# Performance work log

Measured on AMD Instinct MI355X. Metric: run time of the kernel, lower is better.

Reference implementation:

```python
import jax, jax.numpy as jnp
import numpy as np

B, S, H, HEADS, STEP = 128, 256, 128, 8, 1


def setup_inputs() -> dict:
    key = jax.random.key(0)
    ks = jax.random.split(key, 20)
    rn = lambda k, shape: jax.random.normal(k, shape, dtype=jnp.float32) * 0.1
    return {
        "A": jax.random.uniform(ks[0], (B, S, 2 * S), dtype=jnp.float32),
        "hidden": jax.random.normal(ks[1], (B, S, H), dtype=jnp.float32),
        "mask": jnp.ones((B, S), dtype=jnp.int32),
        "w_ih": rn(ks[2], (3 * H, 2 * H)),
        "w_hh": rn(ks[3], (3 * H, H)),
        "b_ih": rn(ks[4], (3 * H,)),
        "b_hh": rn(ks[5], (3 * H,)),
        "b_iah": rn(ks[6], (H,)),
        "b_oah": rn(ks[7], (H,)),
        "W_ein": rn(ks[8], (H, H)), "b_ein": rn(ks[9], (H,)),
        "W_eout": rn(ks[10], (H, H)), "b_eout": rn(ks[11], (H,)),
        "W_q0": rn(ks[12], (H, H)), "b_q0": rn(ks[13], (H,)),
        "W_q1": rn(ks[14], (H, H)), "b_q1": rn(ks[15], (H,)),
        "W_q2": rn(ks[16], (H, H)), "b_q2": rn(ks[17], (H,)),
    }


def _forward(A, hidden, mask, w_ih, w_hh, b_ih, b_hh, b_iah, b_oah,
             W_ein, b_ein, W_eout, b_eout, W_q0, b_q0, W_q1, b_q1, W_q2, b_q2):
    b, s, h = hidden.shape
    dk = h // HEADS
    # ---- GNN: gated graph propagation (GRU cell over adjacency messages) ----
    for _ in range(STEP):
        msg_in = A[:, :, :s] @ (hidden @ W_ein.T + b_ein) + b_iah    # [B,S,H]
        msg_out = A[:, :, s:] @ (hidden @ W_eout.T + b_eout) + b_oah  # [B,S,H]
        inputs = jnp.concatenate([msg_in, msg_out], axis=2)           # [B,S,2H]
        gi = inputs @ w_ih.T + b_ih                                   # [B,S,3H]
        gh = hidden @ w_hh.T + b_hh                                   # [B,S,3H]
        i_r, i_i, i_n = jnp.split(gi, 3, axis=2)
        h_r, h_i, h_n = jnp.split(gh, 3, axis=2)
        resetgate = jax.nn.sigmoid(i_r + h_r)
        inputgate = jax.nn.sigmoid(i_i + h_i)
        newgate = jnp.tanh(i_n + resetgate * h_n)
        hidden = hidden - inputgate * (hidden - newgate)
    # ---- query: hidden state of the last valid item in each session ----
    last_idx = jnp.sum(mask, axis=1) - 1
    ht1 = hidden[jnp.arange(b), last_idx]                             # [B,H]
    # ---- LastAttenion: sigmoid score + double softmax readout ----
    q0 = (ht1 @ W_q0.T + b_q0).reshape(b, HEADS, dk)                  # [B,h,dk]
    q1 = (hidden @ W_q1.T + b_q1).reshape(b, s, HEADS, dk).transpose(0, 2, 1, 3)
    q2 = (hidden @ W_q2.T + b_q2).reshape(b, s, HEADS, dk).transpose(0, 2, 1, 3)
    # q0 is expanded over the query axis, so every score row is identical
    alpha = jax.nn.sigmoid(jnp.einsum('bhd,bhjd->bhj', q0, q1))        # [B,h,S]
    alpha = jnp.broadcast_to(alpha[:, :, None, :], (b, HEADS, s, s))   # [B,h,S,S]
    alpha = jax.nn.softmax(alpha, axis=-1)
    row_keep = (mask > 0)[:, None, :, None]                            # [B,1,S,1]
    alpha = jnp.where(row_keep, alpha, -jnp.inf)
    alpha = jax.nn.softmax(2.0 * alpha, axis=1)                        # over heads
    alpha = jnp.where(row_keep, alpha, 0.0)  # guard fully-masked rows (torch would NaN)
    x = jnp.einsum('bhij,bhjd->bhid', alpha, q2)                       # [B,h,S,dk]
    x = x.transpose(0, 2, 1, 3).reshape(b, s, h)                       # [B,S,H]
    a = jnp.sum(x * mask[:, :, None].astype(x.dtype), axis=1)          # [B,H]
    return a


def reference(A, hidden, mask, w_ih, w_hh, b_ih, b_hh, b_iah, b_oah,
              W_ein, b_ein, W_eout, b_eout, W_q0, b_q0, W_q1, b_q1, W_q2, b_q2):
    return _forward(A, hidden, mask, w_ih, w_hh, b_ih, b_hh, b_iah, b_oah,
                    W_ein, b_ein, W_eout, b_eout, W_q0, b_q0, W_q1, b_q1, W_q2, b_q2)
```

## Files before the change

kernel.cpp:

```cpp
#include <hip/hip_runtime.h>
#include <cstdint>
#include <cstddef>

#define BB   128
#define SS   256
#define HH   128
#define NH   8
#define DKK  16

typedef unsigned short u16;
typedef __attribute__((ext_vector_type(8))) short   sh8;
typedef __attribute__((ext_vector_type(4))) float   f32x4;

__device__ __forceinline__ float sigmoidf_(float x) { return 1.f / (1.f + expf(-x)); }

__device__ __forceinline__ u16 f2bf(float x) {
    union { float f; unsigned int u; } v; v.f = x;
    unsigned int r = (v.u + 0x7fffu + ((v.u >> 16) & 1u)) >> 16;
    return (u16)r;
}
__device__ __forceinline__ float bf2f(u16 u) {
    union { unsigned int u; float f; } v; v.u = ((unsigned int)u) << 16;
    return v.f;
}
__device__ __forceinline__ float bflo(unsigned u) {
    union { unsigned u; float f; } v; v.u = u << 16; return v.f;
}
__device__ __forceinline__ float bfhi(unsigned u) {
    union { unsigned u; float f; } v; v.u = u & 0xffff0000u; return v.f;
}

#define BKk 32
#define PK  40

template<int XMODE, int OMODE>
__global__ __launch_bounds__(256) void gemm_mfma(
    const void* __restrict__ Xa, const void* __restrict__ Xc, int ldx, int ldx1, int ksplit,
    long long sXb, long long sXh,
    const u16* __restrict__ Bw, int ldb, long long sBb, long long sBh,
    const float* __restrict__ bias,
    void* __restrict__ Out, long long ldo, long long sOb, long long sOh,
    int K, const u16* __restrict__ hid)
{
    __shared__ __align__(16) char smem[2 * 128 * PK * 2];
    u16* As = (u16*)smem;
    u16* Bs = (u16*)(smem + 128 * PK * 2);

    const int t  = threadIdx.x;
    const int bm = blockIdx.x * 128;
    const int bn = blockIdx.y * 128;
    const long long zb = blockIdx.z >> 1, zh = blockIdx.z & 1;

    const u16* Bp = Bw + zb * sBb + zh * sBh;

    const int wave = t >> 6, lane = t & 63;
    const int wr = (wave >> 1) * 64, wc = (wave & 1) * 64;
    const int fm = lane & 15, fq = lane >> 4;

    f32x4 acc[4][4] = {};

    const int r0  = t >> 2, kk0 = (t & 3) * 8;
    const int r1  = t >> 3, kk1 = (t & 7) * 4;

    uint4  px0, px1, pb0, pb1;
    float4 pf0, pf1, pf2, pf3;

#define LOADX(K0)                                                                    \
    if (XMODE == 1) {                                                                \
        const float* Xf_ = (const float*)Xa + zb * sXb + zh * sXh;                   \
        const float* xp_ = Xf_ + (long long)(bm + r1) * ldx + (K0) + kk1;            \
        pf0 = *(const float4*)(xp_);                                                 \
        pf1 = *(const float4*)(xp_ + 32LL * ldx);                                    \
        pf2 = *(const float4*)(xp_ + 64LL * ldx);                                    \
        pf3 = *(const float4*)(xp_ + 96LL * ldx);                                    \
    } else if (XMODE == 2 && (K0) >= ksplit) {                                       \
        const u16* xp_ = (const u16*)Xc + (long long)(bm + r0) * ldx1                \
                         + ((K0) - ksplit) + kk0;                                    \
        px0 = *(const uint4*)(xp_);                                                  \
        px1 = *(const uint4*)(xp_ + 64LL * ldx1);                                    \
    } else {                                                                         \
        const u16* xp_ = (const u16*)Xa + (long long)(bm + r0) * ldx + (K0) + kk0;   \
        px0 = *(const uint4*)(xp_);                                                  \
        px1 = *(const uint4*)(xp_ + 64LL * ldx);                                     \
    }

#define LOADB(K0)                                                                    \
    {                                                                                \
        const u16* bp_ = Bp + (long long)(bn + r0) * ldb + (K0) + kk0;               \
        pb0 = *(const uint4*)(bp_);                                                  \
        pb1 = *(const uint4*)(bp_ + 64LL * ldb);                                     \
    }

    LOADX(0)
    LOADB(0)

    for (int k0 = 0; k0 < K; k0 += BKk) {
        if (XMODE == 1) {
            ushort4 w0 = { f2bf(pf0.x), f2bf(pf0.y), f2bf(pf0.z), f2bf(pf0.w) };
            ushort4 w1 = { f2bf(pf1.x), f2bf(pf1.y), f2bf(pf1.z), f2bf(pf1.w) };
            ushort4 w2 = { f2bf(pf2.x), f2bf(pf2.y), f2bf(pf2.z), f2bf(pf2.w) };
            ushort4 w3 = { f2bf(pf3.x), f2bf(pf3.y), f2bf(pf3.z), f2bf(pf3.w) };
            *(ushort4*)&As[(r1     ) * PK + kk1] = w0;
            *(ushort4*)&As[(r1 + 32) * PK + kk1] = w1;
            *(ushort4*)&As[(r1 + 64) * PK + kk1] = w2;
            *(ushort4*)&As[(r1 + 96) * PK + kk1] = w3;
        } else {
            *(uint4*)&As[(r0     ) * PK + kk0] = px0;
            *(uint4*)&As[(r0 + 64) * PK + kk0] = px1;
        }
        *(uint4*)&Bs[(r0     ) * PK + kk0] = pb0;
        *(uint4*)&Bs[(r0 + 64) * PK + kk0] = pb1;
        __syncthreads();

        if (k0 + BKk < K) {
            LOADX(k0 + BKk)
            LOADB(k0 + BKk)
        }

        sh8 af[4], bfr[4];
        #pragma unroll
        for (int i = 0; i < 4; i++) af[i]  = *(const sh8*)&As[(wr + i * 16 + fm) * PK + fq * 8];
        #pragma unroll
        for (int j = 0; j < 4; j++) bfr[j] = *(const sh8*)&Bs[(wc + j * 16 + fm) * PK + fq * 8];
        #pragma unroll
        for (int i = 0; i < 4; i++)
            #pragma unroll
            for (int j = 0; j < 4; j++)
                acc[i][j] = __builtin_amdgcn_mfma_f32_16x16x32_bf16(af[i], bfr[j], acc[i][j], 0, 0, 0);
        __syncthreads();
    }
#undef LOADX
#undef LOADB

    if (OMODE != 3) {
        #pragma unroll
        for (int j = 0; j < 4; j++) {
            const int col = bn + wc + j * 16 + fm;
            const float bj = bias ? bias[col] : 0.f;
            #pragma unroll
            for (int i = 0; i < 4; i++) {
                const int row0 = bm + wr + i * 16 + fq * 4;
                if (OMODE == 1) {
                    u16* O = (u16*)Out + zb * sOb + zh * sOh;
                    #pragma unroll
                    for (int r = 0; r < 4; r++)
                        O[(long long)(row0 + r) * ldo + col] = f2bf(acc[i][j][r] + bj);
                } else {
                    u16* O = (u16*)Out + zb * sOb + zh * sOh;
                    ushort4 w = { f2bf(acc[i][j][0] + bj), f2bf(acc[i][j][1] + bj),
                                  f2bf(acc[i][j][2] + bj), f2bf(acc[i][j][3] + bj) };
                    *(ushort4*)&O[(long long)col * ldo + row0] = w;
                }
            }
        }
    } else {
        float* g4s = (float*)smem;
        const int chbase = bn >> 2;
        const int s_t = t >> 3;
        const int cq  = t & 7;
        u16* O = (u16*)Out;
        const int sbase = (wr ? 16 : 0) + fq * 4;
        #pragma unroll
        for (int i = 0; i < 4; i++) {
            #pragma unroll
            for (int j = 0; j < 4; j++) {
                const int q = wc + j * 16 + fm;
                const float bj = bias[bn + q];
                #pragma unroll
                for (int r = 0; r < 4; r++)
                    g4s[(sbase + r) * 132 + q] = acc[i][j][r] + bj;
            }
            __syncthreads();
            {
                const int grow = bm + i * 16 + (s_t < 16 ? s_t : s_t + 48);
                const ushort4 hv = *(const ushort4*)&hid[(long long)grow * HH + chbase + 4 * cq];
                const float hvv[4] = { bf2f(hv.x), bf2f(hv.y), bf2f(hv.z), bf2f(hv.w) };
                ushort4 w;
                u16* wp = (u16*)&w;
                #pragma unroll
                for (int m = 0; m < 4; m++) {
                    f32x4 gv = *(const f32x4*)&g4s[s_t * 132 + 16 * cq + 4 * m];
                    float rg = sigmoidf_(gv[0]);
                    float ig = sigmoidf_(gv[1]);
                    float ng = tanhf(gv[2] + rg * gv[3]);
                    wp[m] = f2bf(hvv[m] - ig * (hvv[m] - ng));
                }
                *(ushort4*)&O[(long long)grow * ldo + chbase + 4 * cq] = w;
            }
            __syncthreads();
        }
    }
}

__global__ __launch_bounds__(256) void k_prepw(
    const float* __restrict__ hidden, u16* __restrict__ h_bf,
    const float* __restrict__ w_ih, const float* __restrict__ w_hh,
    const float* __restrict__ b_ih, const float* __restrict__ b_hh,
    const float* __restrict__ b_iah, const float* __restrict__ b_oah,
    const float* __restrict__ W_ein, const float* __restrict__ b_ein,
    const float* __restrict__ W_eout, const float* __restrict__ b_eout,
    const float* __restrict__ W_q1, const float* __restrict__ b_q1,
    const float* __restrict__ W_q2, const float* __restrict__ b_q2,
    u16* __restrict__ W2bf, float* __restrict__ bias2,
    u16* __restrict__ Wcat, float* __restrict__ biascat,
    u16* __restrict__ Wq12, float* __restrict__ biasq12)
{
    int idx = blockIdx.x * 256 + threadIdx.x;
    {
        float4 v = ((const float4*)hidden)[idx];
        ushort4 w = { f2bf(v.x), f2bf(v.y), f2bf(v.z), f2bf(v.w) };
        ((ushort4*)h_bf)[idx] = w;
    }
    if (idx < 512 * 384) {
        int np = idx / 384, kk = idx % 384;
        int c = np >> 2, g = np & 3;
        float v;
        if (g < 2)       v = (kk < 256) ? w_ih[(g * 128 + c) * 256 + kk]
                                        : w_hh[(g * 128 + c) * 128 + kk - 256];
        else if (g == 2) v = (kk < 256) ? w_ih[(256 + c) * 256 + kk] : 0.f;
        else             v = (kk < 256) ? 0.f : w_hh[(256 + c) * 128 + kk - 256];
        W2bf[idx] = f2bf(v);
    }
    if (idx < 256 * 128) {
        int n = idx >> 7, k = idx & 127;
        Wcat[idx] = f2bf(n < 128 ? W_ein[n * 128 + k] : W_eout[(n - 128) * 128 + k]);
        Wq12[idx] = f2bf(n < 128 ? W_q1[n * 128 + k]  : W_q2[(n - 128) * 128 + k]);
    }
    if (idx < 512) {
        int np = idx, c = np >> 2, g = np & 3;
        float s;
        if (g < 2)       s = b_ih[g * 128 + c] + b_hh[g * 128 + c];
        else if (g == 2) s = b_ih[256 + c];
        else             s = b_hh[256 + c];
        if (g < 3) {
            int n = (g < 2) ? g * 128 + c : 256 + c;
            for (int k = 0; k < 128; k++)
                s += w_ih[n * 256 + k] * b_iah[k] + w_ih[n * 256 + 128 + k] * b_oah[k];
        }
        bias2[np] = s;
    }
    if (idx < 256) {
        biascat[idx] = idx < 128 ? b_ein[idx] : b_eout[idx - 128];
        biasq12[idx] = idx < 128 ? b_q1[idx]  : b_q2[idx - 128];
    }
}

__global__ __launch_bounds__(1024) void k_tail(
    const u16* __restrict__ hnew_bf, const int* __restrict__ mask,
    const u16* __restrict__ q12, const float* __restrict__ Wq0,
    const float* __restrict__ bq0, float* __restrict__ out)
{
    const int b = blockIdx.x, t = threadIdx.x;
    __shared__ float red[1024];
    __shared__ float hs[HH];
    __shared__ float q0s[HH];
    __shared__ float p_s[NH][SS];
    __shared__ float w_s[NH][SS];
    __shared__ int s_nv;

    if (t < 256) red[t] = (float)mask[b * SS + t];
    __syncthreads();
    for (int off = 128; off > 0; off >>= 1) {
        if (t < off) red[t] += red[t + off];
        __syncthreads();
    }
    if (t == 0) s_nv = (int)red[0];
    __syncthreads();
    const int nv = s_nv;
    const int last = (nv - 1) & (SS - 1);

    if (t < HH) hs[t] = bf2f(hnew_bf[((size_t)b * SS + last) * HH + t]);
    __syncthreads();

    {
        const int n = t & 127, kh = t >> 7;
        const float* w = Wq0 + (size_t)n * HH + kh * 16;
        const float* h = hs + kh * 16;
        float s = 0.f;
        #pragma unroll
        for (int k = 0; k < 16; k++) s += h[k] * w[k];
        red[t] = s;
    }
    __syncthreads();
    if (t < HH) {
        float s = bq0[t];
        #pragma unroll
        for (int kh = 0; kh < 8; kh++) s += red[kh * 128 + t];
        q0s[t] = s;
    }
    __syncthreads();

    {
        const int j = t >> 2, q = t & 3;
        const u16* q1r = q12 + ((size_t)b * SS + j) * 256 + q * 32;
        uint4 va = *(const uint4*)(q1r);
        uint4 vb = *(const uint4*)(q1r + 8);
        uint4 vc = *(const uint4*)(q1r + 16);
        uint4 vd = *(const uint4*)(q1r + 24);
        const float* qa = q0s + q * 32;
        float s0 = qa[0]  * bflo(va.x) + qa[1]  * bfhi(va.x)
                 + qa[2]  * bflo(va.y) + qa[3]  * bfhi(va.y)
                 + qa[4]  * bflo(va.z) + qa[5]  * bfhi(va.z)
                 + qa[6]  * bflo(va.w) + qa[7]  * bfhi(va.w)
                 + qa[8]  * bflo(vb.x) + qa[9]  * bfhi(vb.x)
                 + qa[10] * bflo(vb.y) + qa[11] * bfhi(vb.y)
                 + qa[12] * bflo(vb.z) + qa[13] * bfhi(vb.z)
                 + qa[14] * bflo(vb.w) + qa[15] * bfhi(vb.w);
        float s1 = qa[16] * bflo(vc.x) + qa[17] * bfhi(vc.x)
                 + qa[18] * bflo(vc.y) + qa[19] * bfhi(vc.y)
                 + qa[20] * bflo(vc.z) + qa[21] * bfhi(vc.z)
                 + qa[22] * bflo(vc.w) + qa[23] * bfhi(vc.w)
                 + qa[24] * bflo(vd.x) + qa[25] * bfhi(vd.x)
                 + qa[26] * bflo(vd.y) + qa[27] * bfhi(vd.y)
                 + qa[28] * bflo(vd.z) + qa[29] * bfhi(vd.z)
                 + qa[30] * bflo(vd.w) + qa[31] * bfhi(vd.w);
        p_s[2 * q][j]     = sigmoidf_(s0);
        p_s[2 * q + 1][j] = sigmoidf_(s1);
    }
    __syncthreads();

    if (t < 256) {
        const int h = t >> 5, l = t & 31;
        float v[8], m = -1e30f;
        #pragma unroll
        for (int u = 0; u < 8; u++) { v[u] = p_s[h][l * 8 + u]; m = fmaxf(m, v[u]); }
        #pragma unroll
        for (int msk = 1; msk < 32; msk <<= 1) m = fmaxf(m, __shfl_xor(m, msk, 32));
        float sum = 0.f;
        #pragma unroll
        for (int u = 0; u < 8; u++) { v[u] = expf(v[u] - m); sum += v[u]; }
        #pragma unroll
        for (int msk = 1; msk < 32; msk <<= 1) sum += __shfl_xor(sum, msk, 32);
        const float inv = 1.f / sum;
        #pragma unroll
        for (int u = 0; u < 8; u++) p_s[h][l * 8 + u] = v[u] * inv;
    }
    __syncthreads();

    if (t < 256) {
        float e[NH], den = 0.f;
        #pragma unroll
        for (int h = 0; h < NH; h++) { e[h] = expf(2.f * p_s[h][t]); den += e[h]; }
        const float inv = 1.f / den;
        #pragma unroll
        for (int h = 0; h < NH; h++) w_s[h][t] = e[h] * inv;
    }
    __syncthreads();

    {
        const int col = t & 127, jq = t >> 7;
        const int h = col >> 4;
        const u16* q2b = q12 + (size_t)b * SS * 256 + 128 + col;
        float acc = 0.f;
        #pragma unroll 4
        for (int j = jq * 32; j < jq * 32 + 32; j++)
            acc += w_s[h][j] * bf2f(q2b[(size_t)j * 256]);
        red[t] = acc;
    }
    __syncthreads();
    if (t < HH) {
        float s = 0.f;
        #pragma unroll
        for (int jq = 0; jq < 8; jq++) s += red[jq * 128 + t];
        out[(size_t)b * HH + t] = s * (float)nv;
    }
}

extern "C" void kernel_launch(void* const* d_in, const int* in_sizes, int n_in,
                              void* d_out, int out_size, void* d_ws, size_t ws_size,
                              hipStream_t stream)
{
    const float* A      = (const float*)d_in[0];
    const float* hidden = (const float*)d_in[1];
    const int*   mask   = (const int*)d_in[2];
    const float* w_ih   = (const float*)d_in[3];
    const float* w_hh   = (const float*)d_in[4];
    const float* b_ih   = (const float*)d_in[5];
    const float* b_hh   = (const float*)d_in[6];
    const float* b_iah  = (const float*)d_in[7];
    const float* b_oah  = (const float*)d_in[8];
    const float* W_ein  = (const float*)d_in[9];
    const float* b_ein  = (const float*)d_in[10];
    const float* W_eout = (const float*)d_in[11];
    const float* b_eout = (const float*)d_in[12];
    const float* W_q0   = (const float*)d_in[13];
    const float* b_q0   = (const float*)d_in[14];
    const float* W_q1   = (const float*)d_in[15];
    const float* b_q1   = (const float*)d_in[16];
    const float* W_q2   = (const float*)d_in[17];
    const float* b_q2   = (const float*)d_in[18];
    float* out = (float*)d_out;
    char* ws = (char*)d_ws;

    u16*   Et      = (u16*)(ws + 0);
    u16*   Mbuf    = (u16*)(ws + 16777216);
    u16*   q12bf   = (u16*)(ws + 0);
    u16*   hnew_bf = (u16*)(ws + 33554432);
    u16*   h_bf    = (u16*)(ws + 41943040);
    u16*   W2bf    = (u16*)(ws + 50331648);
    u16*   Wcat    = (u16*)(ws + 50724864);
    u16*   Wq12    = (u16*)(ws + 50790400);
    float* bias2   = (float*)(ws + 50855936);
    float* biascat = (float*)(ws + 50857984);
    float* biasq12 = (float*)(ws + 50859008);

    k_prepw<<<4096, 256, 0, stream>>>(hidden, h_bf,
                                      w_ih, w_hh, b_ih, b_hh, b_iah, b_oah,
                                      W_ein, b_ein, W_eout, b_eout,
                                      W_q1, b_q1, W_q2, b_q2,
                                      W2bf, bias2, Wcat, biascat, Wq12, biasq12);

    gemm_mfma<0, 2><<<dim3(256, 2, 1), 256, 0, stream>>>(
        h_bf, nullptr, HH, 0, 0, 0, 0,
        Wcat, HH, 0, 0, biascat,
        Et, 32768, 0, 0, HH, nullptr);

    gemm_mfma<1, 1><<<dim3(2, 1, 256), 256, 0, stream>>>(
        A, nullptr, 512, 0, 0, 131072LL, 256LL,
        Et, 32768, 256LL, 128LL * 32768LL, nullptr,
        Mbuf, 256, 65536LL, 128LL, SS, nullptr);

    gemm_mfma<2, 3><<<dim3(256, 4, 1), 256, 0, stream>>>(
        Mbuf, h_bf, 256, HH, 256, 0, 0,
        W2bf, 384, 0, 0, bias2,
        hnew_bf, HH, 0, 0, 384, h_bf);

    gemm_mfma<0, 1><<<dim3(256, 2, 1), 256, 0, stream>>>(
        hnew_bf, nullptr, HH, 0, 0, 0, 0,
        Wq12, HH, 0, 0, biasq12,
        q12bf, 256, 0, 0, HH, nullptr);

    k_tail<<<BB, 1024, 0, stream>>>(hnew_bf, mask, q12bf, W_q0, b_q0, out);
}
```

Baseline: 217.8 us.

## Fold edge linear layers into GRU weights and drop the edge-projection GEMM

Uses associativity to fold W_ein/W_eout into the w_ih weights in the prep kernel, so the adjacency GEMM multiplies A directly by a transposed bf16 copy of hidden. The folded-out edge biases come back as per-row sums of A times precomputed vectors u and v. Those row sums are accumulated inside the adjacency GEMM and applied in the GRU epilogue. This removes one GEMM launch and its intermediate buffer round-trip, at the cost of a transpose in the prep kernel, a heavier per-element weight fold, and a different bf16 rounding point.

Result: slower. 222.3 us (+2.0%).

```diff
diff --git a/kernel.cpp b/kernel.cpp
--- a/kernel.cpp
+++ b/kernel.cpp
@@ -29,18 +29,23 @@
 __device__ __forceinline__ float bfhi(unsigned u) {
     union { unsigned u; float f; } v; v.u = u & 0xffff0000u; return v.f;
 }
+__device__ __forceinline__ unsigned pack2(u16 lo, u16 hi) {
+    return (unsigned)lo | ((unsigned)hi << 16);
+}
 
 #define BKk 32
 #define PK  40
 
-template<int XMODE, int OMODE>
+template<int XMODE, int OMODE, int RS>
 __global__ __launch_bounds__(256) void gemm_mfma(
     const void* __restrict__ Xa, const void* __restrict__ Xc, int ldx, int ldx1, int ksplit,
     long long sXb, long long sXh,
     const u16* __restrict__ Bw, int ldb, long long sBb, long long sBh,
     const float* __restrict__ bias,
     void* __restrict__ Out, long long ldo, long long sOb, long long sOh,
-    int K, const u16* __restrict__ hid)
+    int K, const u16* __restrict__ hid,
+    float* __restrict__ rsbuf, const float* __restrict__ ubuf,
+    const float* __restrict__ vbuf)
 {
     __shared__ __align__(16) char smem[2 * 128 * PK * 2];
     u16* As = (u16*)smem;
@@ -64,6 +69,7 @@
 
     uint4  px0, px1, pb0, pb1;
     float4 pf0, pf1, pf2, pf3;
+    float rs0 = 0.f, rs1 = 0.f, rs2 = 0.f, rs3 = 0.f;
 
 #define LOADX(K0)                                                                    \
     if (XMODE == 1) {                                                                \
@@ -96,6 +102,12 @@
 
     for (int k0 = 0; k0 < K; k0 += BKk) {
         if (XMODE == 1) {
+            if (RS) {
+                rs0 += pf0.x + pf0.y + pf0.z + pf0.w;
+                rs1 += pf1.x + pf1.y + pf1.z + pf1.w;
+                rs2 += pf2.x + pf2.y + pf2.z + pf2.w;
+                rs3 += pf3.x + pf3.y + pf3.z + pf3.w;
+            }
             ushort4 w0 = { f2bf(pf0.x), f2bf(pf0.y), f2bf(pf0.z), f2bf(pf0.w) };
             ushort4 w1 = { f2bf(pf1.x), f2bf(pf1.y), f2bf(pf1.z), f2bf(pf1.w) };
             ushort4 w2 = { f2bf(pf2.x), f2bf(pf2.y), f2bf(pf2.z), f2bf(pf2.w) };
@@ -132,7 +144,22 @@
 #undef LOADX
 #undef LOADB
 
-    if (OMODE != 3) {
+    if (XMODE == 1 && RS) {
+        float* rsl = (float*)smem;
+        rsl[(r1     ) * 8 + (t & 7)] = rs0;
+        rsl[(r1 + 32) * 8 + (t & 7)] = rs1;
+        rsl[(r1 + 64) * 8 + (t & 7)] = rs2;
+        rsl[(r1 + 96) * 8 + (t & 7)] = rs3;
+        __syncthreads();
+        if (t < 128) {
+            float s = 0.f;
+            #pragma unroll
+            for (int i2 = 0; i2 < 8; i2++) s += rsl[t * 8 + i2];
+            rsbuf[zh * 32768LL + zb * 256LL + bm + t] = s;
+        }
+    }
+
+    if (OMODE == 1) {
         #pragma unroll
         for (int j = 0; j < 4; j++) {
             const int col = bn + wc + j * 16 + fm;
@@ -140,17 +167,10 @@
             #pragma unroll
             for (int i = 0; i < 4; i++) {
                 const int row0 = bm + wr + i * 16 + fq * 4;
-                if (OMODE == 1) {
-                    u16* O = (u16*)Out + zb * sOb + zh * sOh;
-                    #pragma unroll
-                    for (int r = 0; r < 4; r++)
-                        O[(long long)(row0 + r) * ldo + col] = f2bf(acc[i][j][r] + bj);
-                } else {
-                    u16* O = (u16*)Out + zb * sOb + zh * sOh;
-                    ushort4 w = { f2bf(acc[i][j][0] + bj), f2bf(acc[i][j][1] + bj),
-                                  f2bf(acc[i][j][2] + bj), f2bf(acc[i][j][3] + bj) };
-                    *(ushort4*)&O[(long long)col * ldo + row0] = w;
-                }
+                u16* O = (u16*)Out + zb * sOb + zh * sOh;
+                #pragma unroll
+                for (int r = 0; r < 4; r++)
+                    O[(long long)(row0 + r) * ldo + col] = f2bf(acc[i][j][r] + bj);
             }
         }
     } else {
@@ -158,8 +178,10 @@
         const int chbase = bn >> 2;
         const int s_t = t >> 3;
         const int cq  = t & 7;
+        const int ncol0 = bn + 16 * cq;
         u16* O = (u16*)Out;
         const int sbase = (wr ? 16 : 0) + fq * 4;
+        if (XMODE == 1 && RS) __syncthreads();
         #pragma unroll
         for (int i = 0; i < 4; i++) {
             #pragma unroll
@@ -173,6 +195,8 @@
             __syncthreads();
             {
                 const int grow = bm + i * 16 + (s_t < 16 ? s_t : s_t + 48);
+                const float rin  = rsbuf[grow];
+                const float rout = rsbuf[32768 + grow];
                 const ushort4 hv = *(const ushort4*)&hid[(long long)grow * HH + chbase + 4 * cq];
                 const float hvv[4] = { bf2f(hv.x), bf2f(hv.y), bf2f(hv.z), bf2f(hv.w) };
                 ushort4 w;
@@ -180,9 +204,15 @@
                 #pragma unroll
                 for (int m = 0; m < 4; m++) {
                     f32x4 gv = *(const f32x4*)&g4s[s_t * 132 + 16 * cq + 4 * m];
-                    float rg = sigmoidf_(gv[0]);
-                    float ig = sigmoidf_(gv[1]);
-                    float ng = tanhf(gv[2] + rg * gv[3]);
+                    const float4 um = *(const float4*)&ubuf[ncol0 + 4 * m];
+                    const float4 vm = *(const float4*)&vbuf[ncol0 + 4 * m];
+                    float g0 = gv[0] + rin * um.x + rout * vm.x;
+                    float g1 = gv[1] + rin * um.y + rout * vm.y;
+                    float g2 = gv[2] + rin * um.z + rout * vm.z;
+                    float g3 = gv[3] + rin * um.w + rout * vm.w;
+                    float rg = sigmoidf_(g0);
+                    float ig = sigmoidf_(g1);
+                    float ng = tanhf(g2 + rg * g3);
                     wp[m] = f2bf(hvv[m] - ig * (hvv[m] - ng));
                 }
                 *(ushort4*)&O[(long long)grow * ldo + chbase + 4 * cq] = w;
@@ -193,7 +223,7 @@
 }
 
 __global__ __launch_bounds__(256) void k_prepw(
-    const float* __restrict__ hidden, u16* __restrict__ h_bf,
+    const float* __restrict__ hidden, u16* __restrict__ h_bf, u16* __restrict__ h_bfT,
     const float* __restrict__ w_ih, const float* __restrict__ w_hh,
     const float* __restrict__ b_ih, const float* __restrict__ b_hh,
     const float* __restrict__ b_iah, const float* __restrict__ b_oah,
@@ -201,8 +231,8 @@
     const float* __restrict__ W_eout, const float* __restrict__ b_eout,
     const float* __restrict__ W_q1, const float* __restrict__ b_q1,
     const float* __restrict__ W_q2, const float* __restrict__ b_q2,
-    u16* __restrict__ W2bf, float* __restrict__ bias2,
-    u16* __restrict__ Wcat, float* __restrict__ biascat,
+    u16* __restrict__ W3bf, float* __restrict__ bias2,
+    float* __restrict__ ubuf, float* __restrict__ vbuf,
     u16* __restrict__ Wq12, float* __restrict__ biasq12)
 {
     int idx = blockIdx.x * 256 + threadIdx.x;
@@ -214,17 +244,25 @@
     if (idx < 512 * 384) {
         int np = idx / 384, kk = idx % 384;
         int c = np >> 2, g = np & 3;
-        float v;
-        if (g < 2)       v = (kk < 256) ? w_ih[(g * 128 + c) * 256 + kk]
-                                        : w_hh[(g * 128 + c) * 128 + kk - 256];
-        else if (g == 2) v = (kk < 256) ? w_ih[(256 + c) * 256 + kk] : 0.f;
-        else             v = (kk < 256) ? 0.f : w_hh[(256 + c) * 128 + kk - 256];
-        W2bf[idx] = f2bf(v);
+        float v = 0.f;
+        if (kk >= 256) {
+            if (g < 2)       v = w_hh[(g * 128 + c) * 128 + kk - 256];
+            else if (g == 3) v = w_hh[(256 + c) * 128 + kk - 256];
+        } else if (g != 3) {
+            const int n2 = (g < 2) ? g * 128 + c : 256 + c;
+            const int half = kk >> 7, dd = kk & 127;
+            const float* wr_ = w_ih + n2 * 256 + half * 128;
+            const float* we_ = half ? W_eout : W_ein;
+            float s = 0.f;
+            #pragma unroll 8
+            for (int q = 0; q < 128; q++) s += wr_[q] * we_[q * 128 + dd];
+            v = s;
+        }
+        W3bf[idx] = f2bf(v);
     }
     if (idx < 256 * 128) {
         int n = idx >> 7, k = idx & 127;
-        Wcat[idx] = f2bf(n < 128 ? W_ein[n * 128 + k] : W_eout[(n - 128) * 128 + k]);
-        Wq12[idx] = f2bf(n < 128 ? W_q1[n * 128 + k]  : W_q2[(n - 128) * 128 + k]);
+        Wq12[idx] = f2bf(n < 128 ? W_q1[n * 128 + k] : W_q2[(n - 128) * 128 + k]);
     }
     if (idx < 512) {
         int np = idx, c = np >> 2, g = np & 3;
@@ -232,16 +270,44 @@
         if (g < 2)       s = b_ih[g * 128 + c] + b_hh[g * 128 + c];
         else if (g == 2) s = b_ih[256 + c];
         else             s = b_hh[256 + c];
-        if (g < 3) {
-            int n = (g < 2) ? g * 128 + c : 256 + c;
-            for (int k = 0; k < 128; k++)
-                s += w_ih[n * 256 + k] * b_iah[k] + w_ih[n * 256 + 128 + k] * b_oah[k];
+        float uu = 0.f, vv = 0.f;
+        if (g != 3) {
+            const int n2 = (g < 2) ? g * 128 + c : 256 + c;
+            for (int k = 0; k < 128; k++) {
+                s  += w_ih[n2 * 256 + k] * b_iah[k] + w_ih[n2 * 256 + 128 + k] * b_oah[k];
+                uu += w_ih[n2 * 256 + k] * b_ein[k];
+                vv += w_ih[n2 * 256 + 128 + k] * b_eout[k];
+            }
         }
         bias2[np] = s;
+        ubuf[np] = uu;
+        vbuf[np] = vv;
     }
     if (idx < 256) {
-        biascat[idx] = idx < 128 ? b_ein[idx] : b_eout[idx - 128];
-        biasq12[idx] = idx < 128 ? b_q1[idx]  : b_q2[idx - 128];
+        biasq12[idx] = idx < 128 ? b_q1[idx] : b_q2[idx - 128];
+    }
+    if (blockIdx.x < 512) {
+        const int b = blockIdx.x >> 2, jc = blockIdx.x & 3;
+        const int c = threadIdx.x >> 1, j0 = (threadIdx.x & 1) * 32;
+        const float* src = hidden + ((size_t)b * 256 + jc * 64 + j0) * 128 + c;
+        u16* dst = h_bfT + ((size_t)b * 128 + c) * 256 + jc * 64 + j0;
+        #pragma unroll
+        for (int g8 = 0; g8 < 4; g8++) {
+            float a0 = src[(g8 * 8 + 0) * 128];
+            float a1 = src[(g8 * 8 + 1) * 128];
+            float a2 = src[(g8 * 8 + 2) * 128];
+            float a3 = src[(g8 * 8 + 3) * 128];
+            float a4 = src[(g8 * 8 + 4) * 128];
+            float a5 = src[(g8 * 8 + 5) * 128];
+            float a6 = src[(g8 * 8 + 6) * 128];
+            float a7 = src[(g8 * 8 + 7) * 128];
+            uint4 w;
+            w.x = pack2(f2bf(a0), f2bf(a1));
+            w.y = pack2(f2bf(a2), f2bf(a3));
+            w.z = pack2(f2bf(a4), f2bf(a5));
+            w.w = pack2(f2bf(a6), f2bf(a7));
+            *(uint4*)(dst + g8 * 8) = w;
+        }
     }
 }
 
@@ -392,43 +458,42 @@
     float* out = (float*)d_out;
     char* ws = (char*)d_ws;
 
-    u16*   Et      = (u16*)(ws + 0);
-    u16*   Mbuf    = (u16*)(ws + 16777216);
+    u16*   Mbuf    = (u16*)(ws + 0);
     u16*   q12bf   = (u16*)(ws + 0);
-    u16*   hnew_bf = (u16*)(ws + 33554432);
-    u16*   h_bf    = (u16*)(ws + 41943040);
-    u16*   W2bf    = (u16*)(ws + 50331648);
-    u16*   Wcat    = (u16*)(ws + 50724864);
-    u16*   Wq12    = (u16*)(ws + 50790400);
-    float* bias2   = (float*)(ws + 50855936);
-    float* biascat = (float*)(ws + 50857984);
-    float* biasq12 = (float*)(ws + 50859008);
-
-    k_prepw<<<4096, 256, 0, stream>>>(hidden, h_bf,
+    u16*   hnew_bf = (u16*)(ws + 16777216);
+    u16*   h_bf    = (u16*)(ws + 25165824);
+    u16*   h_bfT   = (u16*)(ws + 33554432);
+    u16*   W3bf    = (u16*)(ws + 41943040);
+    u16*   Wq12    = (u16*)(ws + 42336256);
+    float* bias2   = (float*)(ws + 42401792);
+    float* ubuf    = (float*)(ws + 42403840);
+    float* vbuf    = (float*)(ws + 42405888);
+    float* biasq12 = (float*)(ws + 42407936);
+    float* rsg     = (float*)(ws + 42408960);
+
+    k_prepw<<<4096, 256, 0, stream>>>(hidden, h_bf, h_bfT,
                                       w_ih, w_hh, b_ih, b_hh, b_iah, b_oah,
                                       W_ein, b_ein, W_eout, b_eout,
                                       W_q1, b_q1, W_q2, b_q2,
-                                      W2bf, bias2, Wcat, biascat, Wq12, biasq12);
-
-    gemm_mfma<0, 2><<<dim3(256, 2, 1), 256, 0, stream>>>(
-        h_bf, nullptr, HH, 0, 0, 0, 0,
-        Wcat, HH, 0, 0, biascat,
-        Et, 32768, 0, 0, HH, nullptr);
-
-    gemm_mfma<1, 1><<<dim3(2, 1, 256), 256, 0, stream>>>(
+                                      W3bf, bias2, ubuf, vbuf, Wq12, biasq12);
+
+    gemm_mfma<1, 1, 1><<<dim3(2, 1, 256), 256, 0, stream>>>(
         A, nullptr, 512, 0, 0, 131072LL, 256LL,
-        Et, 32768, 256LL, 128LL * 32768LL, nullptr,
-        Mbuf, 256, 65536LL, 128LL, SS, nullptr);
-
-    gemm_mfma<2, 3><<<dim3(256, 4, 1), 256, 0, stream>>>(
+        h_bfT, 256, 32768LL, 0LL, nullptr,
+        Mbuf, 256, 65536LL, 128LL, SS, nullptr,
+        rsg, nullptr, nullptr);
+
+    gemm_mfma<2, 3, 0><<<dim3(256, 4, 1), 256, 0, stream>>>(
         Mbuf, h_bf, 256, HH, 256, 0, 0,
-        W2bf, 384, 0, 0, bias2,
-        hnew_bf, HH, 0, 0, 384, h_bf);
-
-    gemm_mfma<0, 1><<<dim3(256, 2, 1), 256, 0, stream>>>(
+        W3bf, 384, 0, 0, bias2,
+        hnew_bf, HH, 0, 0, 384, h_bf,
+        rsg, ubuf, vbuf);
+
+    gemm_mfma<0, 1, 0><<<dim3(256, 2, 1), 256, 0, stream>>>(
         hnew_bf, nullptr, HH, 0, 0, 0, 0,
         Wq12, HH, 0, 0, biasq12,
-        q12bf, 256, 0, 0, HH, nullptr);
+        q12bf, 256, 0, 0, HH, nullptr,
+        nullptr, nullptr, nullptr);
 
     k_tail<<<BB, 1024, 0, stream>>>(hnew_bf, mask, q12bf, W_q0, b_q0, out);
 }
```

## Fold q1/q2 projections into tail kernel via associativity, drop q12 GEMM

Applied to the files above, without the earlier changes.

Removes the separate GEMM that projected all hidden states through W_q1 and W_q2. The tail kernel now reassociates the math. It precomputes q0·W_q1 per head so scores come straight from hidden, and it applies W_q2 after the weighted sum over positions, adding the bias scaled by the weight sum. This saves a full B×S×256 GEMM and its workspace round trip. In exchange the tail kernel holds a 64KB LDS tile of hidden per batch and does more serial per-block work with low occupancy (128 blocks of 1024 threads).

Result: slower. 225.2 us (+3.4%).

```diff
diff --git a/kernel.cpp b/kernel.cpp
--- a/kernel.cpp
+++ b/kernel.cpp
@@ -199,11 +199,8 @@
     const float* __restrict__ b_iah, const float* __restrict__ b_oah,
     const float* __restrict__ W_ein, const float* __restrict__ b_ein,
     const float* __restrict__ W_eout, const float* __restrict__ b_eout,
-    const float* __restrict__ W_q1, const float* __restrict__ b_q1,
-    const float* __restrict__ W_q2, const float* __restrict__ b_q2,
     u16* __restrict__ W2bf, float* __restrict__ bias2,
-    u16* __restrict__ Wcat, float* __restrict__ biascat,
-    u16* __restrict__ Wq12, float* __restrict__ biasq12)
+    u16* __restrict__ Wcat, float* __restrict__ biascat)
 {
     int idx = blockIdx.x * 256 + threadIdx.x;
     {
@@ -224,7 +221,6 @@
     if (idx < 256 * 128) {
         int n = idx >> 7, k = idx & 127;
         Wcat[idx] = f2bf(n < 128 ? W_ein[n * 128 + k] : W_eout[(n - 128) * 128 + k]);
-        Wq12[idx] = f2bf(n < 128 ? W_q1[n * 128 + k]  : W_q2[(n - 128) * 128 + k]);
     }
     if (idx < 512) {
         int np = idx, c = np >> 2, g = np & 3;
@@ -241,23 +237,36 @@
     }
     if (idx < 256) {
         biascat[idx] = idx < 128 ? b_ein[idx] : b_eout[idx - 128];
-        biasq12[idx] = idx < 128 ? b_q1[idx]  : b_q2[idx - 128];
     }
 }
 
 __global__ __launch_bounds__(1024) void k_tail(
     const u16* __restrict__ hnew_bf, const int* __restrict__ mask,
-    const u16* __restrict__ q12, const float* __restrict__ Wq0,
-    const float* __restrict__ bq0, float* __restrict__ out)
+    const float* __restrict__ Wq0, const float* __restrict__ bq0,
+    const float* __restrict__ Wq1, const float* __restrict__ bq1,
+    const float* __restrict__ Wq2, const float* __restrict__ bq2,
+    float* __restrict__ out)
 {
     const int b = blockIdx.x, t = threadIdx.x;
+    __shared__ u16   hL[SS * HH];
     __shared__ float red[1024];
-    __shared__ float hs[HH];
     __shared__ float q0s[HH];
+    __shared__ float q0t[NH][HH];
+    __shared__ float cbs[NH];
     __shared__ float p_s[NH][SS];
     __shared__ float w_s[NH][SS];
+    __shared__ float ybuf[NH][HH];
+    __shared__ float swb[NH];
     __shared__ int s_nv;
 
+    const u16* hrow = hnew_bf + (size_t)b * SS * HH;
+
+    {
+        const uint4* src = (const uint4*)hrow;
+        uint4* dst = (uint4*)hL;
+        #pragma unroll
+        for (int i = 0; i < 4; i++) dst[t + 1024 * i] = src[t + 1024 * i];
+    }
     if (t < 256) red[t] = (float)mask[b * SS + t];
     __syncthreads();
     for (int off = 128; off > 0; off >>= 1) {
@@ -269,16 +278,13 @@
     const int nv = s_nv;
     const int last = (nv - 1) & (SS - 1);
 
-    if (t < HH) hs[t] = bf2f(hnew_bf[((size_t)b * SS + last) * HH + t]);
-    __syncthreads();
-
     {
         const int n = t & 127, kh = t >> 7;
         const float* w = Wq0 + (size_t)n * HH + kh * 16;
-        const float* h = hs + kh * 16;
-        float s = 0.f;
-        #pragma unroll
-        for (int k = 0; k < 16; k++) s += h[k] * w[k];
+        const u16* h = hL + last * HH + kh * 16;
+        float s = 0.f;
+        #pragma unroll
+        for (int k = 0; k < 16; k++) s += bf2f(h[k]) * w[k];
         red[t] = s;
     }
     __syncthreads();
@@ -291,31 +297,40 @@
     __syncthreads();
 
     {
-        const int j = t >> 2, q = t & 3;
-        const u16* q1r = q12 + ((size_t)b * SS + j) * 256 + q * 32;
-        uint4 va = *(const uint4*)(q1r);
-        uint4 vb = *(const uint4*)(q1r + 8);
-        uint4 vc = *(const uint4*)(q1r + 16);
-        uint4 vd = *(const uint4*)(q1r + 24);
-        const float* qa = q0s + q * 32;
-        float s0 = qa[0]  * bflo(va.x) + qa[1]  * bfhi(va.x)
-                 + qa[2]  * bflo(va.y) + qa[3]  * bfhi(va.y)
-                 + qa[4]  * bflo(va.z) + qa[5]  * bfhi(va.z)
-                 + qa[6]  * bflo(va.w) + qa[7]  * bfhi(va.w)
-                 + qa[8]  * bflo(vb.x) + qa[9]  * bfhi(vb.x)
-                 + qa[10] * bflo(vb.y) + qa[11] * bfhi(vb.y)
-                 + qa[12] * bflo(vb.z) + qa[13] * bfhi(vb.z)
-                 + qa[14] * bflo(vb.w) + qa[15] * bfhi(vb.w);
-        float s1 = qa[16] * bflo(vc.x) + qa[17] * bfhi(vc.x)
-                 + qa[18] * bflo(vc.y) + qa[19] * bfhi(vc.y)
-                 + qa[20] * bflo(vc.z) + qa[21] * bfhi(vc.z)
-                 + qa[22] * bflo(vc.w) + qa[23] * bfhi(vc.w)
-                 + qa[24] * bflo(vd.x) + qa[25] * bfhi(vd.x)
-                 + qa[26] * bflo(vd.y) + qa[27] * bfhi(vd.y)
-                 + qa[28] * bflo(vd.z) + qa[29] * bfhi(vd.z)
-                 + qa[30] * bflo(vd.w) + qa[31] * bfhi(vd.w);
-        p_s[2 * q][j]     = sigmoidf_(s0);
-        p_s[2 * q + 1][j] = sigmoidf_(s1);
+        const int h = t >> 7, c = t & 127;
+        const float* w = Wq1 + (size_t)(h * 16) * HH + c;
+        float s = 0.f;
+        #pragma unroll
+        for (int d = 0; d < 16; d++) s += q0s[h * 16 + d] * w[(size_t)d * HH];
+        q0t[h][c] = s;
+    }
+    if (t < NH) {
+        float s = 0.f;
+        #pragma unroll
+        for (int d = 0; d < 16; d++) s += q0s[t * 16 + d] * bq1[t * 16 + d];
+        cbs[t] = s;
+    }
+    __syncthreads();
+
+    {
+        const int j = t & 255, hp = t >> 8;
+        const u16* hr = hrow + (size_t)j * HH;
+        const float* qa = &q0t[2 * hp][0];
+        const float* qb = &q0t[2 * hp + 1][0];
+        float s0 = 0.f, s1 = 0.f;
+        #pragma unroll 4
+        for (int c8 = 0; c8 < 16; c8++) {
+            uint4 v = *(const uint4*)(hr + c8 * 8);
+            const int c0 = c8 * 8;
+            float x0 = bflo(v.x), x1 = bfhi(v.x), x2 = bflo(v.y), x3 = bfhi(v.y);
+            float x4 = bflo(v.z), x5 = bfhi(v.z), x6 = bflo(v.w), x7 = bfhi(v.w);
+            s0 += qa[c0] * x0 + qa[c0 + 1] * x1 + qa[c0 + 2] * x2 + qa[c0 + 3] * x3
+                + qa[c0 + 4] * x4 + qa[c0 + 5] * x5 + qa[c0 + 6] * x6 + qa[c0 + 7] * x7;
+            s1 += qb[c0] * x0 + qb[c0 + 1] * x1 + qb[c0 + 2] * x2 + qb[c0 + 3] * x3
+                + qb[c0 + 4] * x4 + qb[c0 + 5] * x5 + qb[c0 + 6] * x6 + qb[c0 + 7] * x7;
+        }
+        p_s[2 * hp][j]     = sigmoidf_(s0 + cbs[2 * hp]);
+        p_s[2 * hp + 1][j] = sigmoidf_(s1 + cbs[2 * hp + 1]);
     }
     __syncthreads();
 
@@ -347,22 +362,32 @@
     }
     __syncthreads();
 
-    {
-        const int col = t & 127, jq = t >> 7;
-        const int h = col >> 4;
-        const u16* q2b = q12 + (size_t)b * SS * 256 + 128 + col;
-        float acc = 0.f;
-        #pragma unroll 4
-        for (int j = jq * 32; j < jq * 32 + 32; j++)
-            acc += w_s[h][j] * bf2f(q2b[(size_t)j * 256]);
-        red[t] = acc;
-    }
-    __syncthreads();
+    if (t < 256) {
+        const int h = t >> 5, l = t & 31;
+        float s = 0.f;
+        #pragma unroll
+        for (int u = 0; u < 8; u++) s += w_s[h][l * 8 + u];
+        #pragma unroll
+        for (int msk = 1; msk < 32; msk <<= 1) s += __shfl_xor(s, msk, 32);
+        if (l == 0) swb[h] = s;
+    }
+
+    {
+        const int h = t >> 7, c = t & 127;
+        float s = 0.f;
+        #pragma unroll 8
+        for (int j = 0; j < 256; j++) s += w_s[h][j] * bf2f(hL[j * HH + c]);
+        ybuf[h][c] = s;
+    }
+    __syncthreads();
+
     if (t < HH) {
-        float s = 0.f;
-        #pragma unroll
-        for (int jq = 0; jq < 8; jq++) s += red[jq * 128 + t];
-        out[(size_t)b * HH + t] = s * (float)nv;
+        const int col = t, h = col >> 4;
+        const float* w = Wq2 + (size_t)col * HH;
+        float s = 0.f;
+        #pragma unroll 8
+        for (int c = 0; c < 128; c++) s += ybuf[h][c] * w[c];
+        out[(size_t)b * HH + col] = (s + bq2[col] * swb[h]) * (float)nv;
     }
 }
 
@@ -394,21 +419,17 @@
 
     u16*   Et      = (u16*)(ws + 0);
     u16*   Mbuf    = (u16*)(ws + 16777216);
-    u16*   q12bf   = (u16*)(ws + 0);
     u16*   hnew_bf = (u16*)(ws + 33554432);
     u16*   h_bf    = (u16*)(ws + 41943040);
     u16*   W2bf    = (u16*)(ws + 50331648);
     u16*   Wcat    = (u16*)(ws + 50724864);
-    u16*   Wq12    = (u16*)(ws + 50790400);
-    float* bias2   = (float*)(ws + 50855936);
-    float* biascat = (float*)(ws + 50857984);
-    float* biasq12 = (float*)(ws + 50859008);
+    float* bias2   = (float*)(ws + 50790400);
+    float* biascat = (float*)(ws + 50792448);
 
     k_prepw<<<4096, 256, 0, stream>>>(hidden, h_bf,
                                       w_ih, w_hh, b_ih, b_hh, b_iah, b_oah,
                                       W_ein, b_ein, W_eout, b_eout,
-                                      W_q1, b_q1, W_q2, b_q2,
-                                      W2bf, bias2, Wcat, biascat, Wq12, biasq12);
+                                      W2bf, bias2, Wcat, biascat);
 
     gemm_mfma<0, 2><<<dim3(256, 2, 1), 256, 0, stream>>>(
         h_bf, nullptr, HH, 0, 0, 0, 0,
@@ -425,10 +446,6 @@
         W2bf, 384, 0, 0, bias2,
         hnew_bf, HH, 0, 0, 384, h_bf);
 
-    gemm_mfma<0, 1><<<dim3(256, 2, 1), 256, 0, stream>>>(
-        hnew_bf, nullptr, HH, 0, 0, 0, 0,
-        Wq12, HH, 0, 0, biasq12,
-        q12bf, 256, 0, 0, HH, nullptr);
-
-    k_tail<<<BB, 1024, 0, stream>>>(hnew_bf, mask, q12bf, W_q0, b_q0, out);
-}
+    k_tail<<<BB, 1024, 0, stream>>>(hnew_bf, mask,
+                                    W_q0, b_q0, W_q1, b_q1, W_q2, b_q2, out);
+}
```
